# Optimization experiments

Hardware: AMD Instinct MI355X
Metric: run time of the kernel (lower is better)

The kernel has to match this reference:

```python
import jax, jax.numpy as jnp
import numpy as np

N, E, C = 25000, 400000, 64
NUM_ELEM, NUM_BESSEL, HID, NPATH, L = 4, 8, 64, 5, 2
R_MAX, AVG_NN = 5.0, 16.0
SQRT3, SQRT2 = 3.0 ** 0.5, 2.0 ** 0.5


def setup_inputs() -> dict:
    key = jax.random.key(0)
    ks = jax.random.split(key, 16)
    def w(k, shape, fan_in):
        return jax.random.normal(k, shape, jnp.float32) / np.float32(np.sqrt(fan_in))
    return {
        "positions": jax.random.normal(ks[0], (N, 3), jnp.float32),
        "species": jax.random.randint(ks[1], (N,), 0, NUM_ELEM, jnp.int32),
        "edge_index": jax.random.randint(ks[2], (2, E), 0, N, jnp.int32),
        "node_embed_W": w(ks[3], (NUM_ELEM, C), NUM_ELEM),
        "lin_up_W0": w(ks[4], (L, C, C), C),
        "lin_up_W1": w(ks[5], (L, C, C), C),
        "mlp_W1": w(ks[6], (L, NUM_BESSEL, HID), NUM_BESSEL),
        "mlp_W2": w(ks[7], (L, HID, HID), HID),
        "mlp_W3": w(ks[8], (L, HID, NPATH * C), HID),
        "lin_W0": w(ks[9], (L, C, C), C),
        "lin_W1": w(ks[10], (L, C, C), C),
        "prod_W0": w(ks[11], (L, NUM_ELEM, 3, C), 3),
        "prod_W1": w(ks[12], (L, NUM_ELEM, 2, C), 2),
        "prod_lin_W0": w(ks[13], (L, C, C), C),
        "prod_lin_W1": w(ks[14], (L, C, C), C),
    }


def _poly_cutoff(r):  # MACE polynomial cutoff, p=6
    p = 6.0
    x = r / R_MAX
    f = (1.0 - 0.5 * (p + 1.0) * (p + 2.0) * x ** 6
         + p * (p + 2.0) * x ** 7 - 0.5 * p * (p + 1.0) * x ** 8)
    return f * (x < 1.0)


def reference(positions, species, edge_index, node_embed_W,
              lin_up_W0, lin_up_W1, mlp_W1, mlp_W2, mlp_W3,
              lin_W0, lin_W1, prod_W0, prod_W1, prod_lin_W0, prod_lin_W1):
    sender, receiver = edge_index[0], edge_index[1]
    vec = positions[sender] - positions[receiver]                  # [E,3]
    r = jnp.maximum(jnp.linalg.norm(vec, axis=-1), 1e-6)           # [E]
    u = vec / r[:, None]
    Y1 = SQRT3 * u                                                 # l=1 SH (component norm); Y0 == 1
    # Bessel radial embedding with polynomial cutoff -> edge_feats [E, NUM_BESSEL]
    n = jnp.arange(1, NUM_BESSEL + 1, dtype=jnp.float32)
    bessel = jnp.sqrt(2.0 / R_MAX) * jnp.sin(n[None, :] * jnp.pi * r[:, None] / R_MAX) / r[:, None]
    edge_feats = bessel * _poly_cutoff(r)[:, None]
    node_attrs = jax.nn.one_hot(species, NUM_ELEM, dtype=jnp.float32)  # [N,4]
    h0 = node_attrs @ node_embed_W                                 # [N,C] scalars
    h1 = jnp.zeros((N, C, 3), jnp.float32)                         # [N,C,3] vectors
    for l in range(L):
        # linear up-projection (per-l channel mixing)
        x0 = h0 @ lin_up_W0[l]
        x1 = jnp.einsum('ncd,ck->nkd', h1, lin_up_W1[l])
        # per-edge radial MLP -> tensor-product path weights [E,5,C]
        tpw = jax.nn.silu(edge_feats @ mlp_W1[l])
        tpw = jax.nn.silu(tpw @ mlp_W2[l])
        tpw = (tpw @ mlp_W3[l]).reshape(E, NPATH, C)
        xs0, xs1 = x0[sender], x1[sender]                          # gather senders
        # CG tensor product (uvu): paths 0x0->0, 0x1->1, 1x0->1, 1x1->0, 1x1->1
        m0 = tpw[:, 0] * xs0 + tpw[:, 3] * (jnp.einsum('ecd,ed->ec', xs1, Y1) / SQRT3)
        m1 = (tpw[:, 1][..., None] * xs0[..., None] * Y1[:, None, :]
              + tpw[:, 2][..., None] * xs1
              + tpw[:, 4][..., None] * jnp.cross(xs1, Y1[:, None, :]) / SQRT2)
        # scatter-sum aggregation over receivers
        M0 = jax.ops.segment_sum(m0, receiver, num_segments=N) / AVG_NN
        M1 = jax.ops.segment_sum(m1, receiver, num_segments=N) / AVG_NN
        h0 = M0 @ lin_W0[l]
        h1 = jnp.einsum('ncd,ck->nkd', M1, lin_W1[l])
        # equivariant product basis (correlation-2 symmetric contraction, element-dependent weights)
        pw0 = jnp.einsum('ne,epc->npc', node_attrs, prod_W0[l])    # [N,3,C]
        paths0 = jnp.stack([h0, h0 * h0, (h1 * h1).sum(-1) / SQRT3], axis=1)
        b0 = (pw0 * paths0).sum(1)
        pw1 = jnp.einsum('ne,epc->npc', node_attrs, prod_W1[l])    # [N,2,C]
        b1 = pw1[:, 0][..., None] * h1 + pw1[:, 1][..., None] * (h0[..., None] * h1)
        h0 = b0 @ prod_lin_W0[l]
        h1 = jnp.einsum('ncd,ck->nkd', b1, prod_lin_W1[l])
    return jnp.concatenate([h0[..., None], h1], axis=-1)           # [N,C,4]
```

## Files before the change

### kernel.cpp

```cpp
#include <hip/hip_runtime.h>
#include <math.h>

#define CDIM 64
#define NBES 8

#define SQRT3_F     1.7320508075688772f
#define INV_SQRT3_F 0.57735026918962576f
#define INV_SQRT2_F 0.70710678118654752f
#define INV_AVG_NN  0.0625f

__device__ __forceinline__ float silu(float x) {
    return x / (1.0f + expf(-x));
}

__global__ __launch_bounds__(256) void k_init(float* __restrict__ h0,
                                              float* __restrict__ h1,
                                              const int* __restrict__ species,
                                              const float* __restrict__ embedW,
                                              int nnodes) {
    int idx = blockIdx.x * 256 + threadIdx.x;
    int n64 = nnodes * 64;
    if (idx < n64) {
        int n = idx >> 6, k = idx & 63;
        h0[idx] = embedW[species[n] * 64 + k];
    } else if (idx < nnodes * 256) {
        h1[idx - n64] = 0.f;
    }
}

__global__ __launch_bounds__(256) void k_linup(float* __restrict__ h0,
                                               float* __restrict__ h1,
                                               const float* __restrict__ W0,
                                               const float* __restrict__ W1,
                                               float* __restrict__ x0,
                                               float* __restrict__ x1,
                                               int nnodes) {
    __shared__ float sh[4][4][64];
    const int w = threadIdx.x >> 6, k = threadIdx.x & 63;
    const int n = blockIdx.x * 4 + w;
    const bool valid = n < nnodes;
    float v0 = valid ? h0[n * 64 + k] : 0.f;
    float v1 = valid ? h1[n * 192 + k] : 0.f;
    float v2 = valid ? h1[n * 192 + 64 + k] : 0.f;
    float v3 = valid ? h1[n * 192 + 128 + k] : 0.f;
    sh[w][0][k] = v0; sh[w][1][k] = v1; sh[w][2][k] = v2; sh[w][3][k] = v3;
    if (valid) {
        h0[n * 64 + k] = 0.f;
        h1[n * 192 + k] = 0.f;
        h1[n * 192 + 64 + k] = 0.f;
        h1[n * 192 + 128 + k] = 0.f;
    }
    __syncthreads();
    float a0 = 0.f, a1 = 0.f, a2 = 0.f, a3 = 0.f;
    for (int c = 0; c < 64; ++c) {
        float w0 = W0[c * 64 + k], w1 = W1[c * 64 + k];
        a0 = fmaf(sh[w][0][c], w0, a0);
        a1 = fmaf(sh[w][1][c], w1, a1);
        a2 = fmaf(sh[w][2][c], w1, a2);
        a3 = fmaf(sh[w][3][c], w1, a3);
    }
    if (valid) {
        x0[n * 64 + k] = a0;
        x1[n * 192 + k] = a1;
        x1[n * 192 + 64 + k] = a2;
        x1[n * 192 + 128 + k] = a3;
    }
}

__global__ __launch_bounds__(320, 4) void k_edge0(
    const float* __restrict__ pos, const int* __restrict__ eidx,
    const float* __restrict__ x0,
    const float* __restrict__ W1, const float* __restrict__ W2,
    const float* __restrict__ W3,
    float* __restrict__ M0, float* __restrict__ M1, int nedges) {
    __shared__ __align__(16) float sFEAT[64][8];
    __shared__ float sY1[64][3];
    __shared__ int sSend[64];
    __shared__ int sRecv[64];
    __shared__ __align__(16) float sH2[64 * 68];
    __shared__ __align__(16) float sU0[4352];

    float* const sH1T = sU0;
    float* const sTP = sU0;

    const int t = threadIdx.x;
    const int wv = t >> 6;

    if (t < 64) {
        int e = blockIdx.x * 64 + t;
        int s = 0, r = 0;
        float y0 = 0.f, y1 = 0.f, y2 = 0.f;
        float feats[NBES];
#pragma unroll
        for (int b = 0; b < NBES; ++b) feats[b] = 0.f;
        if (e < nedges) {
            s = eidx[e];
            r = eidx[nedges + e];
            double dx = (double)pos[3 * s + 0] - (double)pos[3 * r + 0];
            double dy = (double)pos[3 * s + 1] - (double)pos[3 * r + 1];
            double dz = (double)pos[3 * s + 2] - (double)pos[3 * r + 2];
            double rr = sqrt(dx * dx + dy * dy + dz * dz);
            if (rr < 1e-6) rr = 1e-6;
            double inv = 1.0 / rr;
            y0 = (float)(1.7320508075688772 * dx * inv);
            y1 = (float)(1.7320508075688772 * dy * inv);
            y2 = (float)(1.7320508075688772 * dz * inv);
            double xx = rr * 0.2;
            double f = 0.0;
            if (xx < 1.0) {
                double x2 = xx * xx, x3 = x2 * xx, x6 = x3 * x3;
                f = 1.0 - 28.0 * x6 + 48.0 * x6 * xx - 21.0 * x6 * x2;
            }
            double pref = 0.63245553203367587 * f * inv;
#pragma unroll
            for (int b = 0; b < NBES; ++b) {
                double arg = (double)(b + 1) * 3.14159265358979324 * rr * 0.2;
                feats[b] = (float)(sin(arg) * pref);
            }
        }
        sSend[t] = s;
        sRecv[t] = r;
        sY1[t][0] = y0; sY1[t][1] = y1; sY1[t][2] = y2;
#pragma unroll
        for (int b = 0; b < NBES; ++b) sFEAT[t][b] = feats[b];
    }
    __syncthreads();

    if (t < 256) {
        const int j = t & 63;
        float w1c[NBES];
#pragma unroll
        for (int b = 0; b < NBES; ++b) w1c[b] = W1[b * 64 + j];
#pragma unroll
        for (int i = 0; i < 16; ++i) {
            int el = wv * 16 + i;
            const float4* fr = (const float4*)(&sFEAT[el][0]);
            float4 f0 = fr[0], f1 = fr[1];
            float acc = 0.f;
            acc = fmaf(f0.x, w1c[0], acc);
            acc = fmaf(f0.y, w1c[1], acc);
            acc = fmaf(f0.z, w1c[2], acc);
            acc = fmaf(f0.w, w1c[3], acc);
            acc = fmaf(f1.x, w1c[4], acc);
            acc = fmaf(f1.y, w1c[5], acc);
            acc = fmaf(f1.z, w1c[6], acc);
            acc = fmaf(f1.w, w1c[7], acc);
            sH1T[j * 68 + el] = silu(acc);
        }
    }
    __syncthreads();

    if (t < 256) {
        const int eg = t >> 4;
        const int j4 = (t & 15) * 4;
        float a00 = 0.f, a01 = 0.f, a02 = 0.f, a03 = 0.f;
        float a10 = 0.f, a11 = 0.f, a12 = 0.f, a13 = 0.f;
        float a20 = 0.f, a21 = 0.f, a22 = 0.f, a23 = 0.f;
        float a30 = 0.f, a31 = 0.f, a32 = 0.f, a33 = 0.f;
#pragma unroll 4
        for (int k = 0; k < 64; ++k) {
            float4 av = *(const float4*)&sH1T[k * 68 + 4 * eg];
            float4 wv4 = *(const float4*)&W2[k * 64 + j4];
            a00 = fmaf(av.x, wv4.x, a00); a01 = fmaf(av.x, wv4.y, a01);
            a02 = fmaf(av.x, wv4.z, a02); a03 = fmaf(av.x, wv4.w, a03);
            a10 = fmaf(av.y, wv4.x, a10); a11 = fmaf(av.y, wv4.y, a11);
            a12 = fmaf(av.y, wv4.z, a12); a13 = fmaf(av.y, wv4.w, a13);
            a20 = fmaf(av.z, wv4.x, a20); a21 = fmaf(av.z, wv4.y, a21);
            a22 = fmaf(av.z, wv4.z, a22); a23 = fmaf(av.z, wv4.w, a23);
            a30 = fmaf(av.w, wv4.x, a30); a31 = fmaf(av.w, wv4.y, a31);
            a32 = fmaf(av.w, wv4.z, a32); a33 = fmaf(av.w, wv4.w, a33);
        }
        *(float4*)&sH2[(4 * eg + 0) * 68 + j4] =
            make_float4(silu(a00), silu(a01), silu(a02), silu(a03));
        *(float4*)&sH2[(4 * eg + 1) * 68 + j4] =
            make_float4(silu(a10), silu(a11), silu(a12), silu(a13));
        *(float4*)&sH2[(4 * eg + 2) * 68 + j4] =
            make_float4(silu(a20), silu(a21), silu(a22), silu(a23));
        *(float4*)&sH2[(4 * eg + 3) * 68 + j4] =
            make_float4(silu(a30), silu(a31), silu(a32), silu(a33));
    }
    __syncthreads();

    const int eb16 = t & 15;
    const int cb8 = (t >> 4) * 8;
    float acc[4][8];
#pragma unroll
    for (int i = 0; i < 4; ++i)
#pragma unroll
        for (int j = 0; j < 8; ++j) acc[i][j] = 0.f;

    if (t < 256) {
#pragma unroll 1
        for (int kt = 0; kt < 16; ++kt) {
            float4 h[4];
#pragma unroll
            for (int i = 0; i < 4; ++i)
                h[i] = *(const float4*)&sH2[(i * 16 + eb16) * 68 + kt * 4];
#pragma unroll
            for (int kk = 0; kk < 4; ++kk) {
                const int k = kt * 4 + kk;
                float4 wa = *(const float4*)&W3[k * 320 + cb8];
                float4 wb = *(const float4*)&W3[k * 320 + cb8 + 4];
#pragma unroll
                for (int i = 0; i < 4; ++i) {
                    float hv = (kk == 0) ? h[i].x
                             : (kk == 1) ? h[i].y
                             : (kk == 2) ? h[i].z
                                         : h[i].w;
                    acc[i][0] = fmaf(hv, wa.x, acc[i][0]);
                    acc[i][1] = fmaf(hv, wa.y, acc[i][1]);
                    acc[i][2] = fmaf(hv, wa.z, acc[i][2]);
                    acc[i][3] = fmaf(hv, wa.w, acc[i][3]);
                    acc[i][4] = fmaf(hv, wb.x, acc[i][4]);
                    acc[i][5] = fmaf(hv, wb.y, acc[i][5]);
                    acc[i][6] = fmaf(hv, wb.z, acc[i][6]);
                    acc[i][7] = fmaf(hv, wb.w, acc[i][7]);
                }
            }
        }
    }

    const int p0 = cb8 >> 6;
    const int c0 = cb8 & 63;
#pragma unroll
    for (int g = 0; g < 4; ++g) {
        if (t < 256) {
            const int row = (p0 * 16 + eb16) * 68 + c0;
            *(float4*)&sTP[row] =
                make_float4(acc[g][0], acc[g][1], acc[g][2], acc[g][3]);
            *(float4*)&sTP[row + 4] =
                make_float4(acc[g][4], acc[g][5], acc[g][6], acc[g][7]);
        }
        __syncthreads();
        for (int v = t; v < 1024; v += 320) {
            int i = v >> 6, cc = v & 63;
            int el = g * 16 + i;
            int s = sSend[el], r = sRecv[el];
            float X0 = x0[s * 64 + cc];
            float Yx = sY1[el][0], Yy = sY1[el][1], Yz = sY1[el][2];
            float t0 = sTP[(0 * 16 + i) * 68 + cc];
            float t1 = sTP[(1 * 16 + i) * 68 + cc];
            float m0 = t0 * X0;
            float m1 = t1 * X0 * INV_AVG_NN;
            atomicAdd(&M0[r * 64 + cc], m0 * INV_AVG_NN);
            atomicAdd(&M1[r * 192 + cc], m1 * Yx);
            atomicAdd(&M1[r * 192 + 64 + cc], m1 * Yy);
            atomicAdd(&M1[r * 192 + 128 + cc], m1 * Yz);
        }
        __syncthreads();
    }
}

__global__ __launch_bounds__(320, 4) void k_edge(
    const float* __restrict__ pos, const int* __restrict__ eidx,
    const float* __restrict__ x0, const float* __restrict__ x1,
    const float* __restrict__ W1, const float* __restrict__ W2,
    const float* __restrict__ W3,
    float* __restrict__ M0, float* __restrict__ M1, int nedges) {
    __shared__ __align__(16) float sFEAT[64][8];
    __shared__ float sY1[64][3];
    __shared__ int sSend[64];
    __shared__ int sRecv[64];
    __shared__ __align__(16) float sH2[64 * 68];
    __shared__ __align__(16) float sU[5440];

    float* const sH1T = sU;
    float* const sTP = sU;

    const int t = threadIdx.x;
    const int eb = t & 7;
    const int cb8 = (t >> 3) * 8;
    const int wv = t >> 6;
    const int c0 = cb8 & 63;

    if (t < 64) {
        int e = blockIdx.x * 64 + t;
        int s = 0, r = 0;
        float y0 = 0.f, y1 = 0.f, y2 = 0.f;
        float feats[NBES];
#pragma unroll
        for (int b = 0; b < NBES; ++b) feats[b] = 0.f;
        if (e < nedges) {
            s = eidx[e];
            r = eidx[nedges + e];
            double dx = (double)pos[3 * s + 0] - (double)pos[3 * r + 0];
            double dy = (double)pos[3 * s + 1] - (double)pos[3 * r + 1];
            double dz = (double)pos[3 * s + 2] - (double)pos[3 * r + 2];
            double rr = sqrt(dx * dx + dy * dy + dz * dz);
            if (rr < 1e-6) rr = 1e-6;
            double inv = 1.0 / rr;
            y0 = (float)(1.7320508075688772 * dx * inv);
            y1 = (float)(1.7320508075688772 * dy * inv);
            y2 = (float)(1.7320508075688772 * dz * inv);
            double xx = rr * 0.2;
            double f = 0.0;
            if (xx < 1.0) {
                double x2 = xx * xx, x3 = x2 * xx, x6 = x3 * x3;
                f = 1.0 - 28.0 * x6 + 48.0 * x6 * xx - 21.0 * x6 * x2;
            }
            double pref = 0.63245553203367587 * f * inv;
#pragma unroll
            for (int b = 0; b < NBES; ++b) {
                double arg = (double)(b + 1) * 3.14159265358979324 * rr * 0.2;
                feats[b] = (float)(sin(arg) * pref);
            }
        }
        sSend[t] = s;
        sRecv[t] = r;
        sY1[t][0] = y0; sY1[t][1] = y1; sY1[t][2] = y2;
#pragma unroll
        for (int b = 0; b < NBES; ++b) sFEAT[t][b] = feats[b];
    }
    __syncthreads();

    if (t < 256) {
        const int j = t & 63;
        float w1c[NBES];
#pragma unroll
        for (int b = 0; b < NBES; ++b) w1c[b] = W1[b * 64 + j];
#pragma unroll
        for (int i = 0; i < 16; ++i) {
            int el = wv * 16 + i;
            const float4* fr = (const float4*)(&sFEAT[el][0]);
            float4 f0 = fr[0], f1 = fr[1];
            float acc = 0.f;
            acc = fmaf(f0.x, w1c[0], acc);
            acc = fmaf(f0.y, w1c[1], acc);
            acc = fmaf(f0.z, w1c[2], acc);
            acc = fmaf(f0.w, w1c[3], acc);
            acc = fmaf(f1.x, w1c[4], acc);
            acc = fmaf(f1.y, w1c[5], acc);
            acc = fmaf(f1.z, w1c[6], acc);
            acc = fmaf(f1.w, w1c[7], acc);
            sH1T[j * 68 + el] = silu(acc);
        }
    }
    __syncthreads();

    if (t < 256) {
        const int eg = t >> 4;
        const int j4 = (t & 15) * 4;
        float a00 = 0.f, a01 = 0.f, a02 = 0.f, a03 = 0.f;
        float a10 = 0.f, a11 = 0.f, a12 = 0.f, a13 = 0.f;
        float a20 = 0.f, a21 = 0.f, a22 = 0.f, a23 = 0.f;
        float a30 = 0.f, a31 = 0.f, a32 = 0.f, a33 = 0.f;
#pragma unroll 4
        for (int k = 0; k < 64; ++k) {
            float4 av = *(const float4*)&sH1T[k * 68 + 4 * eg];
            float4 wv4 = *(const float4*)&W2[k * 64 + j4];
            a00 = fmaf(av.x, wv4.x, a00); a01 = fmaf(av.x, wv4.y, a01);
            a02 = fmaf(av.x, wv4.z, a02); a03 = fmaf(av.x, wv4.w, a03);
            a10 = fmaf(av.y, wv4.x, a10); a11 = fmaf(av.y, wv4.y, a11);
            a12 = fmaf(av.y, wv4.z, a12); a13 = fmaf(av.y, wv4.w, a13);
            a20 = fmaf(av.z, wv4.x, a20); a21 = fmaf(av.z, wv4.y, a21);
            a22 = fmaf(av.z, wv4.z, a22); a23 = fmaf(av.z, wv4.w, a23);
            a30 = fmaf(av.w, wv4.x, a30); a31 = fmaf(av.w, wv4.y, a31);
            a32 = fmaf(av.w, wv4.z, a32); a33 = fmaf(av.w, wv4.w, a33);
        }
        *(float4*)&sH2[(4 * eg + 0) * 68 + j4] =
            make_float4(silu(a00), silu(a01), silu(a02), silu(a03));
        *(float4*)&sH2[(4 * eg + 1) * 68 + j4] =
            make_float4(silu(a10), silu(a11), silu(a12), silu(a13));
        *(float4*)&sH2[(4 * eg + 2) * 68 + j4] =
            make_float4(silu(a20), silu(a21), silu(a22), silu(a23));
        *(float4*)&sH2[(4 * eg + 3) * 68 + j4] =
            make_float4(silu(a30), silu(a31), silu(a32), silu(a33));
    }
    __syncthreads();

    float acc[8][8];
#pragma unroll
    for (int i = 0; i < 8; ++i)
#pragma unroll
        for (int j = 0; j < 8; ++j) acc[i][j] = 0.f;

#pragma unroll 1
    for (int kt = 0; kt < 16; ++kt) {
        float4 h[8];
#pragma unroll
        for (int i = 0; i < 8; ++i)
            h[i] = *(const float4*)&sH2[(i * 8 + eb) * 68 + kt * 4];
#pragma unroll
        for (int kk = 0; kk < 4; ++kk) {
            const int k = kt * 4 + kk;
            float4 wa = *(const float4*)&W3[k * 320 + cb8];
            float4 wb = *(const float4*)&W3[k * 320 + cb8 + 4];
#pragma unroll
            for (int i = 0; i < 8; ++i) {
                float hv = (kk == 0) ? h[i].x
                         : (kk == 1) ? h[i].y
                         : (kk == 2) ? h[i].z
                                     : h[i].w;
                acc[i][0] = fmaf(hv, wa.x, acc[i][0]);
                acc[i][1] = fmaf(hv, wa.y, acc[i][1]);
                acc[i][2] = fmaf(hv, wa.z, acc[i][2]);
                acc[i][3] = fmaf(hv, wa.w, acc[i][3]);
                acc[i][4] = fmaf(hv, wb.x, acc[i][4]);
                acc[i][5] = fmaf(hv, wb.y, acc[i][5]);
                acc[i][6] = fmaf(hv, wb.z, acc[i][6]);
                acc[i][7] = fmaf(hv, wb.w, acc[i][7]);
            }
        }
    }

#pragma unroll
    for (int g = 0; g < 4; ++g) {
        {
            const int rowA = (wv * 16 + eb) * 68 + c0;
            const int rowB = (wv * 16 + 8 + eb) * 68 + c0;
            *(float4*)&sTP[rowA] =
                make_float4(acc[2 * g][0], acc[2 * g][1], acc[2 * g][2], acc[2 * g][3]);
            *(float4*)&sTP[rowA + 4] =
                make_float4(acc[2 * g][4], acc[2 * g][5], acc[2 * g][6], acc[2 * g][7]);
            *(float4*)&sTP[rowB] =
                make_float4(acc[2 * g + 1][0], acc[2 * g + 1][1], acc[2 * g + 1][2], acc[2 * g + 1][3]);
            *(float4*)&sTP[rowB + 4] =
                make_float4(acc[2 * g + 1][4], acc[2 * g + 1][5], acc[2 * g + 1][6], acc[2 * g + 1][7]);
        }
        __syncthreads();
        for (int v = t; v < 1024; v += 320) {
            int i = v >> 6, cc = v & 63;
            int el = g * 16 + i;
            int s = sSend[el], r = sRecv[el];
            float X0 = x0[s * 64 + cc];
            float Xx = x1[s * 192 + cc];
            float Xy = x1[s * 192 + 64 + cc];
            float Xz = x1[s * 192 + 128 + cc];
            float Yx = sY1[el][0], Yy = sY1[el][1], Yz = sY1[el][2];
            float t0 = sTP[(0 * 16 + i) * 68 + cc];
            float t1 = sTP[(1 * 16 + i) * 68 + cc];
            float t2 = sTP[(2 * 16 + i) * 68 + cc];
            float t3 = sTP[(3 * 16 + i) * 68 + cc];
            float t4 = sTP[(4 * 16 + i) * 68 + cc];
            float dotp = Xx * Yx + Xy * Yy + Xz * Yz;
            float m0 = t0 * X0 + t3 * (dotp * INV_SQRT3_F);
            float cx = Xy * Yz - Xz * Yy;
            float cy = Xz * Yx - Xx * Yz;
            float cz = Xx * Yy - Xy * Yx;
            float m1x = t1 * X0 * Yx + t2 * Xx + t4 * (cx * INV_SQRT2_F);
            float m1y = t1 * X0 * Yy + t2 * Xy + t4 * (cy * INV_SQRT2_F);
            float m1z = t1 * X0 * Yz + t2 * Xz + t4 * (cz * INV_SQRT2_F);
            atomicAdd(&M0[r * 64 + cc], m0 * INV_AVG_NN);
            atomicAdd(&M1[r * 192 + cc], m1x * INV_AVG_NN);
            atomicAdd(&M1[r * 192 + 64 + cc], m1y * INV_AVG_NN);
            atomicAdd(&M1[r * 192 + 128 + cc], m1z * INV_AVG_NN);
        }
        __syncthreads();
    }
}

__global__ __launch_bounds__(256) void k_node(
    float* __restrict__ h0, float* __restrict__ h1,
    const int* __restrict__ species,
    const float* __restrict__ linW0, const float* __restrict__ linW1,
    const float* __restrict__ prodW0, const float* __restrict__ prodW1,
    const float* __restrict__ plinW0, const float* __restrict__ plinW1,
    int nnodes) {
    __shared__ float sh[4][4][64];
    const int w = threadIdx.x >> 6, k = threadIdx.x & 63;
    const int n = blockIdx.x * 4 + w;
    const bool valid = n < nnodes;
    float v0 = valid ? h0[n * 64 + k] : 0.f;
    float v1 = valid ? h1[n * 192 + k] : 0.f;
    float v2 = valid ? h1[n * 192 + 64 + k] : 0.f;
    float v3 = valid ? h1[n * 192 + 128 + k] : 0.f;
    sh[w][0][k] = v0; sh[w][1][k] = v1; sh[w][2][k] = v2; sh[w][3][k] = v3;
    __syncthreads();
    float a0 = 0.f, a1 = 0.f, a2 = 0.f, a3 = 0.f;
    for (int c = 0; c < 64; ++c) {
        float w0 = linW0[c * 64 + k], w1 = linW1[c * 64 + k];
        a0 = fmaf(sh[w][0][c], w0, a0);
        a1 = fmaf(sh[w][1][c], w1, a1);
        a2 = fmaf(sh[w][2][c], w1, a2);
        a3 = fmaf(sh[w][3][c], w1, a3);
    }
    int sp = valid ? species[n] : 0;
    float p00 = prodW0[sp * 192 + k];
    float p01 = prodW0[sp * 192 + 64 + k];
    float p02 = prodW0[sp * 192 + 128 + k];
    float p10 = prodW1[sp * 128 + k];
    float p11 = prodW1[sp * 128 + 64 + k];
    float nsq = a1 * a1 + a2 * a2 + a3 * a3;
    float b0 = p00 * a0 + p01 * (a0 * a0) + p02 * (nsq * INV_SQRT3_F);
    float b1x = p10 * a1 + p11 * (a0 * a1);
    float b1y = p10 * a2 + p11 * (a0 * a2);
    float b1z = p10 * a3 + p11 * (a0 * a3);
    __syncthreads();
    sh[w][0][k] = b0; sh[w][1][k] = b1x; sh[w][2][k] = b1y; sh[w][3][k] = b1z;
    __syncthreads();
    a0 = a1 = a2 = a3 = 0.f;
    for (int c = 0; c < 64; ++c) {
        float w0 = plinW0[c * 64 + k], w1 = plinW1[c * 64 + k];
        a0 = fmaf(sh[w][0][c], w0, a0);
        a1 = fmaf(sh[w][1][c], w1, a1);
        a2 = fmaf(sh[w][2][c], w1, a2);
        a3 = fmaf(sh[w][3][c], w1, a3);
    }
    if (valid) {
        h0[n * 64 + k] = a0;
        h1[n * 192 + k] = a1;
        h1[n * 192 + 64 + k] = a2;
        h1[n * 192 + 128 + k] = a3;
    }
}

__global__ __launch_bounds__(256) void k_out(const float* __restrict__ h0,
                                             const float* __restrict__ h1,
                                             float4* __restrict__ out,
                                             int nnodes) {
    int idx = blockIdx.x * 256 + threadIdx.x;
    if (idx < nnodes * 64) {
        int n = idx >> 6, c = idx & 63;
        float4 o;
        o.x = h0[idx];
        o.y = h1[n * 192 + c];
        o.z = h1[n * 192 + 64 + c];
        o.w = h1[n * 192 + 128 + c];
        out[idx] = o;
    }
}

extern "C" void kernel_launch(void* const* d_in, const int* in_sizes, int n_in,
                              void* d_out, int out_size, void* d_ws,
                              size_t ws_size, hipStream_t stream) {
    const float* positions = (const float*)d_in[0];
    const int* species = (const int*)d_in[1];
    const int* eidx = (const int*)d_in[2];
    const float* embedW = (const float*)d_in[3];
    const float* linupW0 = (const float*)d_in[4];
    const float* linupW1 = (const float*)d_in[5];
    const float* mlpW1 = (const float*)d_in[6];
    const float* mlpW2 = (const float*)d_in[7];
    const float* mlpW3 = (const float*)d_in[8];
    const float* linW0 = (const float*)d_in[9];
    const float* linW1 = (const float*)d_in[10];
    const float* prodW0 = (const float*)d_in[11];
    const float* prodW1 = (const float*)d_in[12];
    const float* plinW0 = (const float*)d_in[13];
    const float* plinW1 = (const float*)d_in[14];

    const int nn = in_sizes[0] / 3;
    const int ne = in_sizes[2] / 2;

    float* h0 = (float*)d_ws;
    float* h1 = h0 + (size_t)nn * 64;
    float* x0 = h1 + (size_t)nn * 192;
    float* x1 = x0 + (size_t)nn * 64;

    const int gridN64 = (nn * 64 + 255) / 256;
    const int gridInit = (nn * 256 + 255) / 256;
    const int gridNode = (nn + 3) / 4;
    const int gridEdge = (ne + 63) / 64;

    k_init<<<gridInit, 256, 0, stream>>>(h0, h1, species, embedW, nn);

    k_linup<<<gridNode, 256, 0, stream>>>(
        h0, h1, linupW0, linupW1, x0, x1, nn);
    k_edge0<<<gridEdge, 320, 0, stream>>>(
        positions, eidx, x0, mlpW1, mlpW2, mlpW3, h0, h1, ne);
    k_node<<<gridNode, 256, 0, stream>>>(
        h0, h1, species, linW0, linW1, prodW0, prodW1, plinW0, plinW1, nn);

    k_linup<<<gridNode, 256, 0, stream>>>(
        h0, h1, linupW0 + 4096, linupW1 + 4096, x0, x1, nn);
    k_edge<<<gridEdge, 320, 0, stream>>>(
        positions, eidx, x0, x1, mlpW1 + 512, mlpW2 + 4096,
        mlpW3 + 20480, h0, h1, ne);
    k_node<<<gridNode, 256, 0, stream>>>(
        h0, h1, species, linW0 + 4096, linW1 + 4096,
        prodW0 + 768, prodW1 + 512, plinW0 + 4096, plinW1 + 4096, nn);

    k_out<<<gridN64, 256, 0, stream>>>(h0, h1, (float4*)d_out, nn);
}
```

Baseline: 1.197 ms.

## Fuse node-wise kernels: init+linup, node+next linup, final node+output

Merges the embedding init and the first linear-up into one kernel that computes x0 straight from the species embedding row. The node update is fused with the next layer's linear-up, zeroing the accumulators in place, and the last node update writes the float4 output directly. This removes three launches and several full passes over the node-feature buffers. The fused node kernel does more work per block and adds an extra shared-memory stage.

```diff
diff --git a/kernel.cpp b/kernel.cpp
--- a/kernel.cpp
+++ b/kernel.cpp
@@ -13,58 +13,21 @@
     return x / (1.0f + expf(-x));
 }
 
-__global__ __launch_bounds__(256) void k_init(float* __restrict__ h0,
-                                              float* __restrict__ h1,
-                                              const int* __restrict__ species,
-                                              const float* __restrict__ embedW,
-                                              int nnodes) {
-    int idx = blockIdx.x * 256 + threadIdx.x;
-    int n64 = nnodes * 64;
-    if (idx < n64) {
-        int n = idx >> 6, k = idx & 63;
-        h0[idx] = embedW[species[n] * 64 + k];
-    } else if (idx < nnodes * 256) {
-        h1[idx - n64] = 0.f;
-    }
-}
-
-__global__ __launch_bounds__(256) void k_linup(float* __restrict__ h0,
-                                               float* __restrict__ h1,
-                                               const float* __restrict__ W0,
-                                               const float* __restrict__ W1,
-                                               float* __restrict__ x0,
-                                               float* __restrict__ x1,
-                                               int nnodes) {
-    __shared__ float sh[4][4][64];
+__global__ __launch_bounds__(256) void k_lin0(
+    float* __restrict__ h0, float* __restrict__ h1,
+    const int* __restrict__ species, const float* __restrict__ embedW,
+    const float* __restrict__ W0, float* __restrict__ x0, int nnodes) {
     const int w = threadIdx.x >> 6, k = threadIdx.x & 63;
     const int n = blockIdx.x * 4 + w;
-    const bool valid = n < nnodes;
-    float v0 = valid ? h0[n * 64 + k] : 0.f;
-    float v1 = valid ? h1[n * 192 + k] : 0.f;
-    float v2 = valid ? h1[n * 192 + 64 + k] : 0.f;
-    float v3 = valid ? h1[n * 192 + 128 + k] : 0.f;
-    sh[w][0][k] = v0; sh[w][1][k] = v1; sh[w][2][k] = v2; sh[w][3][k] = v3;
-    if (valid) {
-        h0[n * 64 + k] = 0.f;
-        h1[n * 192 + k] = 0.f;
-        h1[n * 192 + 64 + k] = 0.f;
-        h1[n * 192 + 128 + k] = 0.f;
-    }
-    __syncthreads();
-    float a0 = 0.f, a1 = 0.f, a2 = 0.f, a3 = 0.f;
-    for (int c = 0; c < 64; ++c) {
-        float w0 = W0[c * 64 + k], w1 = W1[c * 64 + k];
-        a0 = fmaf(sh[w][0][c], w0, a0);
-        a1 = fmaf(sh[w][1][c], w1, a1);
-        a2 = fmaf(sh[w][2][c], w1, a2);
-        a3 = fmaf(sh[w][3][c], w1, a3);
-    }
-    if (valid) {
-        x0[n * 64 + k] = a0;
-        x1[n * 192 + k] = a1;
-        x1[n * 192 + 64 + k] = a2;
-        x1[n * 192 + 128 + k] = a3;
-    }
+    if (n >= nnodes) return;
+    const float* er = embedW + species[n] * 64;
+    float a0 = 0.f;
+    for (int c = 0; c < 64; ++c) a0 = fmaf(er[c], W0[c * 64 + k], a0);
+    x0[n * 64 + k] = a0;
+    h0[n * 64 + k] = 0.f;
+    h1[n * 192 + k] = 0.f;
+    h1[n * 192 + 64 + k] = 0.f;
+    h1[n * 192 + 128 + k] = 0.f;
 }
 
 __global__ __launch_bounds__(320, 4) void k_edge0(
@@ -449,13 +412,14 @@
     }
 }
 
-__global__ __launch_bounds__(256) void k_node(
+__global__ __launch_bounds__(256) void k_nodelin(
     float* __restrict__ h0, float* __restrict__ h1,
     const int* __restrict__ species,
     const float* __restrict__ linW0, const float* __restrict__ linW1,
     const float* __restrict__ prodW0, const float* __restrict__ prodW1,
     const float* __restrict__ plinW0, const float* __restrict__ plinW1,
-    int nnodes) {
+    const float* __restrict__ lupW0, const float* __restrict__ lupW1,
+    float* __restrict__ x0, float* __restrict__ x1, int nnodes) {
     __shared__ float sh[4][4][64];
     const int w = threadIdx.x >> 6, k = threadIdx.x & 63;
     const int n = blockIdx.x * 4 + w;
@@ -465,6 +429,12 @@
     float v2 = valid ? h1[n * 192 + 64 + k] : 0.f;
     float v3 = valid ? h1[n * 192 + 128 + k] : 0.f;
     sh[w][0][k] = v0; sh[w][1][k] = v1; sh[w][2][k] = v2; sh[w][3][k] = v3;
+    if (valid) {
+        h0[n * 64 + k] = 0.f;
+        h1[n * 192 + k] = 0.f;
+        h1[n * 192 + 64 + k] = 0.f;
+        h1[n * 192 + 128 + k] = 0.f;
+    }
     __syncthreads();
     float a0 = 0.f, a1 = 0.f, a2 = 0.f, a3 = 0.f;
     for (int c = 0; c < 64; ++c) {
@@ -496,28 +466,73 @@
         a2 = fmaf(sh[w][2][c], w1, a2);
         a3 = fmaf(sh[w][3][c], w1, a3);
     }
+    __syncthreads();
+    sh[w][0][k] = a0; sh[w][1][k] = a1; sh[w][2][k] = a2; sh[w][3][k] = a3;
+    __syncthreads();
+    a0 = a1 = a2 = a3 = 0.f;
+    for (int c = 0; c < 64; ++c) {
+        float w0 = lupW0[c * 64 + k], w1 = lupW1[c * 64 + k];
+        a0 = fmaf(sh[w][0][c], w0, a0);
+        a1 = fmaf(sh[w][1][c], w1, a1);
+        a2 = fmaf(sh[w][2][c], w1, a2);
+        a3 = fmaf(sh[w][3][c], w1, a3);
+    }
     if (valid) {
-        h0[n * 64 + k] = a0;
-        h1[n * 192 + k] = a1;
-        h1[n * 192 + 64 + k] = a2;
-        h1[n * 192 + 128 + k] = a3;
-    }
-}
-
-__global__ __launch_bounds__(256) void k_out(const float* __restrict__ h0,
-                                             const float* __restrict__ h1,
-                                             float4* __restrict__ out,
-                                             int nnodes) {
-    int idx = blockIdx.x * 256 + threadIdx.x;
-    if (idx < nnodes * 64) {
-        int n = idx >> 6, c = idx & 63;
-        float4 o;
-        o.x = h0[idx];
-        o.y = h1[n * 192 + c];
-        o.z = h1[n * 192 + 64 + c];
-        o.w = h1[n * 192 + 128 + c];
-        out[idx] = o;
-    }
+        x0[n * 64 + k] = a0;
+        x1[n * 192 + k] = a1;
+        x1[n * 192 + 64 + k] = a2;
+        x1[n * 192 + 128 + k] = a3;
+    }
+}
+
+__global__ __launch_bounds__(256) void k_nodeout(
+    const float* __restrict__ h0, const float* __restrict__ h1,
+    const int* __restrict__ species,
+    const float* __restrict__ linW0, const float* __restrict__ linW1,
+    const float* __restrict__ prodW0, const float* __restrict__ prodW1,
+    const float* __restrict__ plinW0, const float* __restrict__ plinW1,
+    float4* __restrict__ out, int nnodes) {
+    __shared__ float sh[4][4][64];
+    const int w = threadIdx.x >> 6, k = threadIdx.x & 63;
+    const int n = blockIdx.x * 4 + w;
+    const bool valid = n < nnodes;
+    float v0 = valid ? h0[n * 64 + k] : 0.f;
+    float v1 = valid ? h1[n * 192 + k] : 0.f;
+    float v2 = valid ? h1[n * 192 + 64 + k] : 0.f;
+    float v3 = valid ? h1[n * 192 + 128 + k] : 0.f;
+    sh[w][0][k] = v0; sh[w][1][k] = v1; sh[w][2][k] = v2; sh[w][3][k] = v3;
+    __syncthreads();
+    float a0 = 0.f, a1 = 0.f, a2 = 0.f, a3 = 0.f;
+    for (int c = 0; c < 64; ++c) {
+        float w0 = linW0[c * 64 + k], w1 = linW1[c * 64 + k];
+        a0 = fmaf(sh[w][0][c], w0, a0);
+        a1 = fmaf(sh[w][1][c], w1, a1);
+        a2 = fmaf(sh[w][2][c], w1, a2);
+        a3 = fmaf(sh[w][3][c], w1, a3);
+    }
+    int sp = valid ? species[n] : 0;
+    float p00 = prodW0[sp * 192 + k];
+    float p01 = prodW0[sp * 192 + 64 + k];
+    float p02 = prodW0[sp * 192 + 128 + k];
+    float p10 = prodW1[sp * 128 + k];
+    float p11 = prodW1[sp * 128 + 64 + k];
+    float nsq = a1 * a1 + a2 * a2 + a3 * a3;
+    float b0 = p00 * a0 + p01 * (a0 * a0) + p02 * (nsq * INV_SQRT3_F);
+    float b1x = p10 * a1 + p11 * (a0 * a1);
+    float b1y = p10 * a2 + p11 * (a0 * a2);
+    float b1z = p10 * a3 + p11 * (a0 * a3);
+    __syncthreads();
+    sh[w][0][k] = b0; sh[w][1][k] = b1x; sh[w][2][k] = b1y; sh[w][3][k] = b1z;
+    __syncthreads();
+    a0 = a1 = a2 = a3 = 0.f;
+    for (int c = 0; c < 64; ++c) {
+        float w0 = plinW0[c * 64 + k], w1 = plinW1[c * 64 + k];
+        a0 = fmaf(sh[w][0][c], w0, a0);
+        a1 = fmaf(sh[w][1][c], w1, a1);
+        a2 = fmaf(sh[w][2][c], w1, a2);
+        a3 = fmaf(sh[w][3][c], w1, a3);
+    }
+    if (valid) out[n * 64 + k] = make_float4(a0, a1, a2, a3);
 }
 
 extern "C" void kernel_launch(void* const* d_in, const int* in_sizes, int n_in,
@@ -547,28 +562,24 @@
     float* x0 = h1 + (size_t)nn * 192;
     float* x1 = x0 + (size_t)nn * 64;
 
-    const int gridN64 = (nn * 64 + 255) / 256;
-    const int gridInit = (nn * 256 + 255) / 256;
     const int gridNode = (nn + 3) / 4;
     const int gridEdge = (ne + 63) / 64;
 
-    k_init<<<gridInit, 256, 0, stream>>>(h0, h1, species, embedW, nn);
-
-    k_linup<<<gridNode, 256, 0, stream>>>(
-        h0, h1, linupW0, linupW1, x0, x1, nn);
+    k_lin0<<<gridNode, 256, 0, stream>>>(
+        h0, h1, species, embedW, linupW0, x0, nn);
     k_edge0<<<gridEdge, 320, 0, stream>>>(
         positions, eidx, x0, mlpW1, mlpW2, mlpW3, h0, h1, ne);
-    k_node<<<gridNode, 256, 0, stream>>>(
-        h0, h1, species, linW0, linW1, prodW0, prodW1, plinW0, plinW1, nn);
-
-    k_linup<<<gridNode, 256, 0, stream>>>(
-        h0, h1, linupW0 + 4096, linupW1 + 4096, x0, x1, nn);
+
+    k_nodelin<<<gridNode, 256, 0, stream>>>(
+        h0, h1, species, linW0, linW1, prodW0, prodW1, plinW0, plinW1,
+        linupW0 + 4096, linupW1 + 4096, x0, x1, nn);
+
     k_edge<<<gridEdge, 320, 0, stream>>>(
         positions, eidx, x0, x1, mlpW1 + 512, mlpW2 + 4096,
         mlpW3 + 20480, h0, h1, ne);
-    k_node<<<gridNode, 256, 0, stream>>>(
+
+    k_nodeout<<<gridNode, 256, 0, stream>>>(
         h0, h1, species, linW0 + 4096, linW1 + 4096,
-        prodW0 + 768, prodW1 + 512, plinW0 + 4096, plinW1 + 4096, nn);
-
-    k_out<<<gridN64, 256, 0, stream>>>(h0, h1, (float4*)d_out, nn);
-}
+        prodW0 + 768, prodW1 + 512, plinW0 + 4096, plinW1 + 4096,
+        (float4*)d_out, nn);
+}
```

Result: faster. 1.170 ms (-2.2%).
